# Kernel tuning notes

Hardware: AMD Instinct MI355X
Metric: run time of the kernel (lower is better)

The kernel has to match this reference:

```python
import jax, jax.numpy as jnp
import numpy as np


def setup_inputs() -> dict:
    key = jax.random.key(0)
    ks = jax.random.split(key, 10)
    B, C, H, W = 4, 64, 96, 96
    C8 = C // 8
    R = C // 16  # CBAM reduction ratio 16
    s = 0.05
    return {
        "x": jax.random.normal(ks[0], (B, C, H, W), dtype=jnp.float32),
        "wq": jax.random.normal(ks[1], (C8, C), dtype=jnp.float32) * s,
        "bq": jnp.zeros((C8,), dtype=jnp.float32),
        "wk": jax.random.normal(ks[2], (C8, C), dtype=jnp.float32) * s,
        "bk": jnp.zeros((C8,), dtype=jnp.float32),
        "wv": jax.random.normal(ks[3], (C, C), dtype=jnp.float32) * s,
        "bv": jnp.zeros((C,), dtype=jnp.float32),
        "ca_w1": jax.random.normal(ks[4], (R, C), dtype=jnp.float32) * s,
        "ca_w2": jax.random.normal(ks[5], (C, R), dtype=jnp.float32) * s,
    }


def reference(x, wq, bq, wk, bk, wv, bv, ca_w1, ca_w2):
    B, C, H, W = x.shape
    N = H * W
    # 1x1 convs as channel einsums
    q = jnp.einsum('bchw,oc->bohw', x, wq) + bq[None, :, None, None]  # [B,C/8,H,W]
    k = jnp.einsum('bchw,oc->bohw', x, wk) + bk[None, :, None, None]
    v = jnp.einsum('bchw,oc->bohw', x, wv) + bv[None, :, None, None]  # [B,C,H,W]
    Q = q.reshape(B, -1, N)          # [B,C8,N]
    K = k.reshape(B, -1, N)          # [B,C8,N]
    V = v.reshape(B, C, N)           # [B,C,N]
    energy = jnp.einsum('bcn,bcm->bnm', Q, K)   # [B,N,N] = Q^T K
    att = jax.nn.sigmoid(energy)
    # out = V @ att^T  -> out[b,c,n] = sum_m V[b,c,m] * att[b,n,m]
    out = jnp.einsum('bcm,bnm->bcn', V, att).reshape(B, C, H, W)
    out = out + x
    # CBAM channel attention: shared bias-free MLP on avg & max pooled features
    avg = out.mean(axis=(2, 3))      # [B,C]
    mx = out.max(axis=(2, 3))        # [B,C]
    def mlp(f):
        h = jax.nn.relu(jnp.einsum('bc,rc->br', f, ca_w1))
        return jnp.einsum('br,cr->bc', h, ca_w2)
    scale = jax.nn.sigmoid(mlp(avg) + mlp(mx))  # [B,C]
    return out * scale[:, :, None, None]
```

## Files before the change

### kernel.cpp

```cpp
#include <hip/hip_runtime.h>
#include <hip/hip_bf16.h>

#define B_  4
#define C_  64
#define C8_ 8
#define N_  9216
#define BN  128
#define BM  64
#define MSPLIT 4
#define MCHUNK (N_ / MSPLIT)
#define NITER  (MCHUNK / BM)
#define NEG_LOG2E (-1.44269504088896340736f)

typedef _Float16 half8  __attribute__((ext_vector_type(8)));
typedef float    f32x16 __attribute__((ext_vector_type(16)));

static __device__ __forceinline__ float fast_exp2(float x){ float r; asm("v_exp_f32 %0, %1":"=v"(r):"v"(x)); return r; }
static __device__ __forceinline__ float fast_rcp (float x){ float r; asm("v_rcp_f32 %0, %1":"=v"(r):"v"(x)); return r; }

static __device__ __forceinline__ void gload16(const void* g, void* l){
    __builtin_amdgcn_global_load_lds((const __attribute__((address_space(1))) void*)g,
                                     (__attribute__((address_space(3))) void*)l, 16, 0, 0);
}

__global__ __launch_bounds__(256) void qkv2_kernel(
        const float* __restrict__ x,
        const float* __restrict__ wq, const float* __restrict__ bq,
        const float* __restrict__ wk, const float* __restrict__ bk,
        const float* __restrict__ wv, const float* __restrict__ bv,
        _Float16* __restrict__ Qt, _Float16* __restrict__ Kt,
        _Float16* __restrict__ Vp) {
    const int tid = threadIdx.x;
    const int wv_i = tid >> 6, lane = tid & 63, l31 = lane & 31, hi = lane >> 5;
    const int b = blockIdx.y;
    const int n = blockIdx.x * 128 + wv_i * 32 + l31;

    half8 af[3][4];
    #pragma unroll
    for (int mt = 0; mt < 3; ++mt) {
        const int o = mt * 32 + l31;
        #pragma unroll
        for (int kk = 0; kk < 4; ++kk) {
            half8 a;
            #pragma unroll
            for (int j = 0; j < 8; ++j) {
                const int c = kk * 16 + hi * 8 + j;
                float v = 0.f;
                if (o < 8)       v = wq[o * C_ + c] * NEG_LOG2E;
                else if (o < 16) v = wk[(o - 8) * C_ + c];
                else if (o < 80) v = wv[(o - 16) * C_ + c];
                a[j] = (_Float16)v;
            }
            af[mt][kk] = a;
        }
    }
    half8 bf[4];
    #pragma unroll
    for (int kk = 0; kk < 4; ++kk) {
        half8 t;
        #pragma unroll
        for (int j = 0; j < 8; ++j) {
            const int c = kk * 16 + hi * 8 + j;
            t[j] = (_Float16)x[(size_t)(b * C_ + c) * N_ + n];
        }
        bf[kk] = t;
    }
    const int low = n & 15;
    const int g2 = (low >> 2) & 3;
    const int low2 = (g2 == 1) ? low + 4 : (g2 == 2) ? low - 4 : low;
    const int posn = (n & ~15) | low2;

    #pragma unroll
    for (int mt = 0; mt < 3; ++mt) {
        f32x16 acc = (f32x16)(0.f);
        #pragma unroll
        for (int kk = 0; kk < 4; ++kk)
            acc = __builtin_amdgcn_mfma_f32_32x32x16_f16(af[mt][kk], bf[kk], acc, 0, 0, 0);
        #pragma unroll
        for (int r = 0; r < 16; ++r) {
            const int o = mt * 32 + (r & 3) + 8 * (r >> 2) + 4 * hi;
            if (o < 8)
                Qt[((size_t)(b * N_) + n) * 8 + o] = (_Float16)(acc[r] + bq[o] * NEG_LOG2E);
            else if (o < 16)
                Kt[((size_t)(b * N_) + n) * 8 + (o - 8)] = (_Float16)(acc[r] + bk[o - 8]);
            else if (o < 80)
                Vp[(size_t)(b * C_ + (o - 16)) * N_ + posn] = (_Float16)(acc[r] + bv[o - 16]);
        }
    }
}

#define VOFF 0
#define KOFF 16384
#define QOFF 18432
#define ZOFF 20480
#define LDSBYTES 20608

#define STAGE(mt, bsel) do {                                                            \
    const int m0s_ = mbase + (mt) * 64;                                                 \
    if (wave == 0)                                                                      \
        gload16(Kt + ((size_t)(b * N_ + m0s_) + lane) * 8, lds + KOFF + (bsel) * 1024); \
    {                                                                                   \
        const int ld0_ = wave * 2;                                                      \
        const int cl0_ = ld0_ * 8 + (lane >> 3);                                        \
        const int q0_  = (lane & 7) ^ (cl0_ & 7);                                       \
        gload16(Vp + (size_t)(b * C_ + cl0_) * N_ + m0s_ + q0_ * 8,                     \
                lds + VOFF + (bsel) * 8192 + ld0_ * 1024);                              \
        const int cl1_ = cl0_ + 8;                                                      \
        const int q1_  = (lane & 7) ^ (cl1_ & 7);                                       \
        gload16(Vp + (size_t)(b * C_ + cl1_) * N_ + m0s_ + q1_ * 8,                     \
                lds + VOFF + (bsel) * 8192 + (ld0_ + 1) * 1024);                        \
    } } while (0)

__global__ __launch_bounds__(256) void attn_kernel(
        const _Float16* __restrict__ Qt, const _Float16* __restrict__ Kt,
        const _Float16* __restrict__ Vp, float* __restrict__ part) {
    __shared__ ulong2 ldsq[LDSBYTES / 16];
    char* lds = (char*)ldsq;
    const int tid  = threadIdx.x;
    const int wave = tid >> 6, lane = tid & 63;
    const int l31  = lane & 31;
    const int hi   = lane >> 5;
    const int b    = blockIdx.z, mh = blockIdx.y;
    const int n0   = blockIdx.x * 128;
    const int mbase = mh * MCHUNK;

    if (tid < 8) ((short*)(lds + ZOFF))[tid] = 0;

    STAGE(0, 0);
    if (wave == 1) {
        gload16(Qt + ((size_t)(b * N_ + n0) + lane) * 8,      lds + QOFF);
        gload16(Qt + ((size_t)(b * N_ + n0 + 64) + lane) * 8, lds + QOFF + 1024);
    }
    __syncthreads();

    const int qa = (lane < 32) ? (QOFF + (wave * 32 + l31) * 16) : ZOFF;
    const half8 qf = *(const half8*)(lds + qa);

    f32x16 acc0 = (f32x16)(0.f), acc1 = (f32x16)(0.f);

    for (int t = 0; t < NITER; ++t) {
        const int buf = t & 1;
        if (t + 1 < NITER) STAGE(t + 1, buf ^ 1);

        const int ka0 = (lane < 32) ? (KOFF + buf * 1024 +       l31 * 16) : ZOFF;
        const int ka1 = (lane < 32) ? (KOFF + buf * 1024 + 512 + l31 * 16) : ZOFF;
        const half8 kf0 = *(const half8*)(lds + ka0);
        const half8 kf1 = *(const half8*)(lds + ka1);
        f32x16 s0 = __builtin_amdgcn_mfma_f32_32x32x16_f16(kf0, qf, (f32x16)(0.f), 0, 0, 0);
        f32x16 s1 = __builtin_amdgcn_mfma_f32_32x32x16_f16(kf1, qf, (f32x16)(0.f), 0, 0, 0);

        #pragma unroll
        for (int r = 0; r < 16; ++r) s0[r] = fast_rcp(1.f + fast_exp2(s0[r]));
        #pragma unroll
        for (int r = 0; r < 16; ++r) s1[r] = fast_rcp(1.f + fast_exp2(s1[r]));

        const int vbase = VOFF + buf * 8192;
        #pragma unroll
        for (int ks = 0; ks < 4; ++ks) {
            f32x16 am = (ks < 2) ? s0 : s1;
            const int bb = (ks & 1) * 8;
            uint4 pk;
            pk.x = __builtin_bit_cast(unsigned int, __builtin_amdgcn_cvt_pkrtz(am[bb + 0], am[bb + 1]));
            pk.y = __builtin_bit_cast(unsigned int, __builtin_amdgcn_cvt_pkrtz(am[bb + 2], am[bb + 3]));
            pk.z = __builtin_bit_cast(unsigned int, __builtin_amdgcn_cvt_pkrtz(am[bb + 4], am[bb + 5]));
            pk.w = __builtin_bit_cast(unsigned int, __builtin_amdgcn_cvt_pkrtz(am[bb + 6], am[bb + 7]));
            const half8 bf = __builtin_bit_cast(half8, pk);
            const int sw = ((2 * ks + hi) ^ (l31 & 7)) * 16;
            const half8 af0 = *(const half8*)(lds + vbase + l31 * 128 + sw);
            const half8 af1 = *(const half8*)(lds + vbase + (32 + l31) * 128 + sw);
            acc0 = __builtin_amdgcn_mfma_f32_32x32x16_f16(af0, bf, acc0, 0, 0, 0);
            acc1 = __builtin_amdgcn_mfma_f32_32x32x16_f16(af1, bf, acc1, 0, 0, 0);
        }
        __syncthreads();
    }

    float* pp = part + ((size_t)(mh * B_ + b) * C_) * (size_t)N_ + n0 + wave * 32 + l31;
    #pragma unroll
    for (int r = 0; r < 16; ++r) {
        const int c0 = (r & 3) + 8 * (r >> 2) + 4 * hi;
        pp[(size_t)c0 * N_]        = acc0[r];
        pp[(size_t)(c0 + 32) * N_] = acc1[r];
    }
}

__global__ void reduce_pool(const float* __restrict__ part, const float* __restrict__ x,
                            float* __restrict__ outp,
                            float* __restrict__ avgP, float* __restrict__ maxP) {
    const int c = blockIdx.x, b = blockIdx.y;
    const size_t off = (size_t)(b * C_ + c) * N_;
    const float4* p0 = (const float4*)(part + ((size_t)(0 * B_ + b) * C_ + c) * N_);
    const float4* p1 = (const float4*)(part + ((size_t)(1 * B_ + b) * C_ + c) * N_);
    const float4* p2 = (const float4*)(part + ((size_t)(2 * B_ + b) * C_ + c) * N_);
    const float4* p3 = (const float4*)(part + ((size_t)(3 * B_ + b) * C_ + c) * N_);
    const float4* xr = (const float4*)(x + off);
    float4* orow = (float4*)(outp + off);
    const int tid = threadIdx.x;
    float s = 0.f, mx = -3.4e38f;
    for (int i = tid; i < N_ / 4; i += 256) {
        float4 a = p0[i], bq = p1[i], cq = p2[i], dq = p3[i], xv = xr[i];
        float4 o;
        o.x = a.x + bq.x + cq.x + dq.x + xv.x;
        o.y = a.y + bq.y + cq.y + dq.y + xv.y;
        o.z = a.z + bq.z + cq.z + dq.z + xv.z;
        o.w = a.w + bq.w + cq.w + dq.w + xv.w;
        orow[i] = o;
        s += o.x + o.y + o.z + o.w;
        mx = fmaxf(mx, fmaxf(fmaxf(o.x, o.y), fmaxf(o.z, o.w)));
    }
    #pragma unroll
    for (int offm = 32; offm > 0; offm >>= 1) {
        s += __shfl_down(s, offm, 64);
        mx = fmaxf(mx, __shfl_down(mx, offm, 64));
    }
    __shared__ float ss[4], sm[4];
    if ((tid & 63) == 0) { ss[tid >> 6] = s; sm[tid >> 6] = mx; }
    __syncthreads();
    if (tid == 0) {
        float fs = ss[0] + ss[1] + ss[2] + ss[3];
        float fm = fmaxf(fmaxf(sm[0], sm[1]), fmaxf(sm[2], sm[3]));
        avgP[b * C_ + c] = fs / (float)N_;
        maxP[b * C_ + c] = fm;
    }
}

__global__ void mlp_kernel(const float* __restrict__ avgP, const float* __restrict__ maxP,
                           const float* __restrict__ w1, const float* __restrict__ w2,
                           float* __restrict__ scaleP) {
    __shared__ float h[32];
    const int tid = threadIdx.x;
    if (tid < 32) {
        int b = tid >> 3, r = (tid >> 1) & 3, wh = tid & 1;
        const float* src = wh ? maxP : avgP;
        float s = 0.f;
        for (int c = 0; c < C_; ++c) s += src[b * C_ + c] * w1[r * C_ + c];
        h[tid] = fmaxf(s, 0.f);
    }
    __syncthreads();
    int b = tid >> 6, c = tid & 63;
    float s = 0.f;
    #pragma unroll
    for (int r = 0; r < 4; ++r)
        s += (h[b * 8 + r * 2] + h[b * 8 + r * 2 + 1]) * w2[c * 4 + r];
    scaleP[tid] = fast_rcp(1.f + fast_exp2(s * NEG_LOG2E));
}

__global__ void scale_kernel(float* __restrict__ outp, const float* __restrict__ scaleP) {
    int i4 = blockIdx.x * 256 + threadIdx.x;
    float sc = scaleP[i4 / (N_ / 4)];
    float4 v = *(const float4*)&outp[(size_t)i4 * 4];
    v.x *= sc; v.y *= sc; v.z *= sc; v.w *= sc;
    *(float4*)&outp[(size_t)i4 * 4] = v;
}

extern "C" void kernel_launch(void* const* d_in, const int* in_sizes, int n_in,
                              void* d_out, int out_size, void* d_ws, size_t ws_size,
                              hipStream_t stream) {
    const float* x  = (const float*)d_in[0];
    const float* wq = (const float*)d_in[1];
    const float* bq = (const float*)d_in[2];
    const float* wk = (const float*)d_in[3];
    const float* bk = (const float*)d_in[4];
    const float* wv = (const float*)d_in[5];
    const float* bv = (const float*)d_in[6];
    const float* w1 = (const float*)d_in[7];
    const float* w2 = (const float*)d_in[8];
    float* outp = (float*)d_out;

    char* w = (char*)d_ws;
    _Float16* Qt = (_Float16*)(w);
    _Float16* Kt = (_Float16*)(w + 589824);
    _Float16* Vp = (_Float16*)(w + 1179648);
    float* part  = (float*)(w + 5898240);
    float* avgP  = (float*)(w + 43646976);
    float* maxP  = avgP + 256;
    float* scaleP = maxP + 256;

    qkv2_kernel<<<dim3(N_ / 128, B_), 256, 0, stream>>>(x, wq, bq, wk, bk, wv, bv, Qt, Kt, Vp);
    attn_kernel<<<dim3(N_ / 128, MSPLIT, B_), 256, 0, stream>>>(Qt, Kt, Vp, part);
    reduce_pool<<<dim3(C_, B_), 256, 0, stream>>>(part, x, outp, avgP, maxP);
    mlp_kernel<<<1, 256, 0, stream>>>(avgP, maxP, w1, w2, scaleP);
    scale_kernel<<<(B_ * C_ * N_ / 4) / 256, 256, 0, stream>>>(outp, scaleP);
}
```

Measured before the change: 210.7 us.

## Split attention over more key chunks, batch sigmoid reciprocals, prepack QKV weights

```diff
diff --git a/kernel.cpp b/kernel.cpp
--- a/kernel.cpp
+++ b/kernel.cpp
@@ -3,13 +3,9 @@
 
 #define B_  4
 #define C_  64
-#define C8_ 8
 #define N_  9216
 #define BN  128
 #define BM  64
-#define MSPLIT 4
-#define MCHUNK (N_ / MSPLIT)
-#define NITER  (MCHUNK / BM)
 #define NEG_LOG2E (-1.44269504088896340736f)
 
 typedef _Float16 half8  __attribute__((ext_vector_type(8)));
@@ -23,11 +19,45 @@
                                      (__attribute__((address_space(3))) void*)l, 16, 0, 0);
 }
 
+static __device__ __forceinline__ void sigmoid16(f32x16& s) {
+    float d[16];
+    #pragma unroll
+    for (int r = 0; r < 16; ++r) d[r] = 1.f + fast_exp2(s[r]);
+    #pragma unroll
+    for (int g = 0; g < 16; g += 8) {
+        const float p1 = d[g+0]*d[g+1], p2 = p1*d[g+2], p3 = p2*d[g+3];
+        const float p4 = p3*d[g+4], p5 = p4*d[g+5], p6 = p5*d[g+6], p7 = p6*d[g+7];
+        const float r7 = fast_rcp(p7);
+        s[g+7] = r7*p6; const float r6 = r7*d[g+7];
+        s[g+6] = r6*p5; const float r5 = r6*d[g+6];
+        s[g+5] = r5*p4; const float r4 = r5*d[g+5];
+        s[g+4] = r4*p3; const float r3 = r4*d[g+4];
+        s[g+3] = r3*p2; const float r2 = r3*d[g+3];
+        s[g+2] = r2*p1; const float r1 = r2*d[g+2];
+        s[g+1] = r1*d[g+0];
+        s[g+0] = r1*d[g+1];
+    }
+}
+
+__global__ void prep_w(const float* __restrict__ wq, const float* __restrict__ wk,
+                       const float* __restrict__ wv, _Float16* __restrict__ Wprep) {
+    for (int t = threadIdx.x; t < 12 * 64 * 8; t += 256) {
+        const int j = t & 7, lane = (t >> 3) & 63, g = t >> 9;
+        const int kk = g & 3, mt = g >> 2;
+        const int o = mt * 32 + (lane & 31);
+        const int c = kk * 16 + (lane >> 5) * 8 + j;
+        float v = 0.f;
+        if (o < 8)       v = wq[o * C_ + c] * NEG_LOG2E;
+        else if (o < 16) v = wk[(o - 8) * C_ + c];
+        else if (o < 80) v = wv[(o - 16) * C_ + c];
+        Wprep[t] = (_Float16)v;
+    }
+}
+
 __global__ __launch_bounds__(256) void qkv2_kernel(
-        const float* __restrict__ x,
-        const float* __restrict__ wq, const float* __restrict__ bq,
-        const float* __restrict__ wk, const float* __restrict__ bk,
-        const float* __restrict__ wv, const float* __restrict__ bv,
+        const float* __restrict__ x, const _Float16* __restrict__ Wprep,
+        const float* __restrict__ bq, const float* __restrict__ bk,
+        const float* __restrict__ bv,
         _Float16* __restrict__ Qt, _Float16* __restrict__ Kt,
         _Float16* __restrict__ Vp) {
     const int tid = threadIdx.x;
@@ -35,25 +65,6 @@
     const int b = blockIdx.y;
     const int n = blockIdx.x * 128 + wv_i * 32 + l31;
 
-    half8 af[3][4];
-    #pragma unroll
-    for (int mt = 0; mt < 3; ++mt) {
-        const int o = mt * 32 + l31;
-        #pragma unroll
-        for (int kk = 0; kk < 4; ++kk) {
-            half8 a;
-            #pragma unroll
-            for (int j = 0; j < 8; ++j) {
-                const int c = kk * 16 + hi * 8 + j;
-                float v = 0.f;
-                if (o < 8)       v = wq[o * C_ + c] * NEG_LOG2E;
-                else if (o < 16) v = wk[(o - 8) * C_ + c];
-                else if (o < 80) v = wv[(o - 16) * C_ + c];
-                a[j] = (_Float16)v;
-            }
-            af[mt][kk] = a;
-        }
-    }
     half8 bf[4];
     #pragma unroll
     for (int kk = 0; kk < 4; ++kk) {
@@ -74,8 +85,10 @@
     for (int mt = 0; mt < 3; ++mt) {
         f32x16 acc = (f32x16)(0.f);
         #pragma unroll
-        for (int kk = 0; kk < 4; ++kk)
-            acc = __builtin_amdgcn_mfma_f32_32x32x16_f16(af[mt][kk], bf[kk], acc, 0, 0, 0);
+        for (int kk = 0; kk < 4; ++kk) {
+            const half8 af = *(const half8*)&Wprep[(((size_t)mt * 4 + kk) * 64 + lane) * 8];
+            acc = __builtin_amdgcn_mfma_f32_32x32x16_f16(af, bf[kk], acc, 0, 0, 0);
+        }
         #pragma unroll
         for (int r = 0; r < 16; ++r) {
             const int o = mt * 32 + (r & 3) + 8 * (r >> 2) + 4 * hi;
@@ -111,9 +124,12 @@
                 lds + VOFF + (bsel) * 8192 + (ld0_ + 1) * 1024);                        \
     } } while (0)
 
+template <int MSP>
 __global__ __launch_bounds__(256) void attn_kernel(
         const _Float16* __restrict__ Qt, const _Float16* __restrict__ Kt,
         const _Float16* __restrict__ Vp, float* __restrict__ part) {
+    constexpr int MCHUNK = N_ / MSP;
+    constexpr int NITER  = MCHUNK / BM;
     __shared__ ulong2 ldsq[LDSBYTES / 16];
     char* lds = (char*)ldsq;
     const int tid  = threadIdx.x;
@@ -149,10 +165,8 @@
         f32x16 s0 = __builtin_amdgcn_mfma_f32_32x32x16_f16(kf0, qf, (f32x16)(0.f), 0, 0, 0);
         f32x16 s1 = __builtin_amdgcn_mfma_f32_32x32x16_f16(kf1, qf, (f32x16)(0.f), 0, 0, 0);
 
-        #pragma unroll
-        for (int r = 0; r < 16; ++r) s0[r] = fast_rcp(1.f + fast_exp2(s0[r]));
-        #pragma unroll
-        for (int r = 0; r < 16; ++r) s1[r] = fast_rcp(1.f + fast_exp2(s1[r]));
+        sigmoid16(s0);
+        sigmoid16(s1);
 
         const int vbase = VOFF + buf * 8192;
         #pragma unroll
@@ -183,26 +197,23 @@
     }
 }
 
+template <int MSP>
 __global__ void reduce_pool(const float* __restrict__ part, const float* __restrict__ x,
                             float* __restrict__ outp,
                             float* __restrict__ avgP, float* __restrict__ maxP) {
     const int c = blockIdx.x, b = blockIdx.y;
     const size_t off = (size_t)(b * C_ + c) * N_;
-    const float4* p0 = (const float4*)(part + ((size_t)(0 * B_ + b) * C_ + c) * N_);
-    const float4* p1 = (const float4*)(part + ((size_t)(1 * B_ + b) * C_ + c) * N_);
-    const float4* p2 = (const float4*)(part + ((size_t)(2 * B_ + b) * C_ + c) * N_);
-    const float4* p3 = (const float4*)(part + ((size_t)(3 * B_ + b) * C_ + c) * N_);
     const float4* xr = (const float4*)(x + off);
     float4* orow = (float4*)(outp + off);
     const int tid = threadIdx.x;
     float s = 0.f, mx = -3.4e38f;
     for (int i = tid; i < N_ / 4; i += 256) {
-        float4 a = p0[i], bq = p1[i], cq = p2[i], dq = p3[i], xv = xr[i];
-        float4 o;
-        o.x = a.x + bq.x + cq.x + dq.x + xv.x;
-        o.y = a.y + bq.y + cq.y + dq.y + xv.y;
-        o.z = a.z + bq.z + cq.z + dq.z + xv.z;
-        o.w = a.w + bq.w + cq.w + dq.w + xv.w;
+        float4 o = xr[i];
+        #pragma unroll
+        for (int m = 0; m < MSP; ++m) {
+            const float4 p = ((const float4*)(part + ((size_t)(m * B_ + b) * C_ + c) * N_))[i];
+            o.x += p.x; o.y += p.y; o.z += p.z; o.w += p.w;
+        }
         orow[i] = o;
         s += o.x + o.y + o.z + o.w;
         mx = fmaxf(mx, fmaxf(fmaxf(o.x, o.y), fmaxf(o.z, o.w)));
@@ -271,13 +282,24 @@
     _Float16* Kt = (_Float16*)(w + 589824);
     _Float16* Vp = (_Float16*)(w + 1179648);
     float* part  = (float*)(w + 5898240);
-    float* avgP  = (float*)(w + 43646976);
-    float* maxP  = avgP + 256;
+    const size_t PART1 = (size_t)B_ * C_ * N_ * 4;
+
+    const int msp = (ws_size >= 5898240 + 8 * PART1 + 16384) ? 8 : 4;
+    char* tail = w + 5898240 + (size_t)msp * PART1;
+    float* avgP = (float*)tail;
+    float* maxP = avgP + 256;
     float* scaleP = maxP + 256;
-
-    qkv2_kernel<<<dim3(N_ / 128, B_), 256, 0, stream>>>(x, wq, bq, wk, bk, wv, bv, Qt, Kt, Vp);
-    attn_kernel<<<dim3(N_ / 128, MSPLIT, B_), 256, 0, stream>>>(Qt, Kt, Vp, part);
-    reduce_pool<<<dim3(C_, B_), 256, 0, stream>>>(part, x, outp, avgP, maxP);
+    _Float16* Wprep = (_Float16*)(tail + 3072);
+
+    prep_w<<<1, 256, 0, stream>>>(wq, wk, wv, Wprep);
+    qkv2_kernel<<<dim3(N_ / 128, B_), 256, 0, stream>>>(x, Wprep, bq, bk, bv, Qt, Kt, Vp);
+    if (msp == 8) {
+        attn_kernel<8><<<dim3(N_ / 128, 8, B_), 256, 0, stream>>>(Qt, Kt, Vp, part);
+        reduce_pool<8><<<dim3(C_, B_), 256, 0, stream>>>(part, x, outp, avgP, maxP);
+    } else {
+        attn_kernel<4><<<dim3(N_ / 128, 4, B_), 256, 0, stream>>>(Qt, Kt, Vp, part);
+        reduce_pool<4><<<dim3(C_, B_), 256, 0, stream>>>(part, x, outp, avgP, maxP);
+    }
     mlp_kernel<<<1, 256, 0, stream>>>(avgP, maxP, w1, w2, scaleP);
     scale_kernel<<<(B_ * C_ * N_ / 4) / 256, 256, 0, stream>>>(outp, scaleP);
 }
```

Measured after the change: 201.2 us. 1.05x faster.
